# Performance work log

Measured on AMD Instinct MI355X. Metric: run time of the kernel, lower is better.

Reference implementation:

```python
import jax, jax.numpy as jnp
import numpy as np

B, CIN, COUT, H, W = 8, 128, 256, 64, 64
EPS = 1e-5


def conv2d(x, w, b, pad):
    y = jax.lax.conv_general_dilated(
        x, w, window_strides=(1, 1), padding=[(pad, pad), (pad, pad)],
        dimension_numbers=('NCHW', 'OIHW', 'NCHW'))
    return y + b[None, :, None, None]


def deform_sample(x, offset):
    # x: [B,C,H,W], offset: [B,18,H,W] -> sampled: [B,C,9,H,W]
    b, c, h, w = x.shape
    off = offset.reshape(b, 9, 2, h, w)  # (dy, dx) per kernel tap (torchvision v1 order)
    ky = (jnp.arange(9) // 3 - 1).astype(x.dtype)
    kx = (jnp.arange(9) % 3 - 1).astype(x.dtype)
    py = jnp.arange(h, dtype=x.dtype)[None, None, :, None] + ky[None, :, None, None] + off[:, :, 0]
    px = jnp.arange(w, dtype=x.dtype)[None, None, None, :] + kx[None, :, None, None] + off[:, :, 1]
    y0 = jnp.floor(py); x0 = jnp.floor(px)
    fy = py - y0;       fx = px - x0
    xf = x.reshape(b, c, h * w)

    def gather(iy, ix):
        valid = (iy >= 0) & (iy < h) & (ix >= 0) & (ix < w)
        iyc = jnp.clip(iy, 0, h - 1).astype(jnp.int32)
        ixc = jnp.clip(ix, 0, w - 1).astype(jnp.int32)
        idx = (iyc * w + ixc).reshape(b, -1)  # [B, 9*H*W]
        g = jax.vmap(lambda xb, ib: jnp.take(xb, ib, axis=1))(xf, idx)  # [B,C,9HW]
        return g.reshape(b, c, 9, h, w) * valid.astype(x.dtype)[:, None]

    samp = (gather(y0,     x0    ) * ((1 - fy) * (1 - fx))[:, None]
          + gather(y0,     x0 + 1) * ((1 - fy) * fx      )[:, None]
          + gather(y0 + 1, x0    ) * (fy * (1 - fx)      )[:, None]
          + gather(y0 + 1, x0 + 1) * (fy * fx            )[:, None])
    return samp


def setup_inputs():
    key = jax.random.key(0)
    ks = jax.random.split(key, 8)
    return {
        'x':     jax.random.normal(ks[0], (B, CIN, H, W), jnp.float32),
        'w_off': jax.random.normal(ks[1], (18, CIN, 3, 3), jnp.float32) * 0.01,
        'b_off': jnp.zeros((18,), jnp.float32),
        'w_def': jax.random.normal(ks[2], (COUT, CIN, 3, 3), jnp.float32) * 0.03,
        'b_def': jax.random.normal(ks[3], (COUT,), jnp.float32) * 0.01,
        'gamma': jnp.ones((COUT,), jnp.float32),
        'beta':  jnp.zeros((COUT,), jnp.float32),
        'w_sc':  jax.random.normal(ks[4], (COUT, CIN, 1, 1), jnp.float32) * 0.05,
        'b_sc':  jnp.zeros((COUT,), jnp.float32),
    }


def reference(x, w_off, b_off, w_def, b_def, gamma, beta, w_sc, b_sc):
    offset = conv2d(x, w_off, b_off, pad=1)                 # [B,18,H,W]
    samp = deform_sample(x, offset)                         # [B,C,9,H,W]
    out = jnp.einsum('bckhw,ock->bohw', samp, w_def.reshape(COUT, CIN, 9))
    out = out + b_def[None, :, None, None]
    # BatchNorm2d (training mode: batch statistics)
    mean = out.mean(axis=(0, 2, 3))
    var = out.var(axis=(0, 2, 3))
    out = (out - mean[None, :, None, None]) * jax.lax.rsqrt(var + EPS)[None, :, None, None]
    out = out * gamma[None, :, None, None] + beta[None, :, None, None]
    out = out + conv2d(x, w_sc, b_sc, pad=0)                # residual shortcut (1x1)
    return jax.nn.relu(out)
```

## Files before the change

kernel.cpp:

```cpp
#include <hip/hip_runtime.h>

typedef __attribute__((ext_vector_type(8))) short bf16x8;
typedef __attribute__((ext_vector_type(4))) float f32x4;

__device__ __forceinline__ float bf2f(unsigned short u) {
  return __uint_as_float(((unsigned int)u) << 16);
}
__device__ __forceinline__ unsigned short f2bf(float f) {
  unsigned int u = __float_as_uint(f);
  u += 0x7fffu + ((u >> 16) & 1u);
  return (unsigned short)(u >> 16);
}

constexpr size_t OFF_XPAD = 0;
constexpr size_t SZ_XPAD  = (size_t)8 * 66 * 66 * 128 * 2;
constexpr size_t OFF_WB   = OFF_XPAD + SZ_XPAD;
constexpr size_t SZ_WB    = (size_t)9 * 16 * 256 * 8 * 2;
constexpr size_t OFF_WS2  = OFF_WB + SZ_WB;
constexpr size_t SZ_WS2   = (size_t)16 * 256 * 8 * 2;
constexpr size_t OFF_WO   = OFF_WS2 + SZ_WS2;
constexpr size_t SZ_WO    = (size_t)9 * 16 * 32 * 8 * 2;
constexpr size_t OFF_OFFS = OFF_WO + SZ_WO;
constexpr size_t SZ_OFFS  = (size_t)9 * 32768 * 2 * 4;
constexpr size_t OFF_YM   = OFF_OFFS + SZ_OFFS;
constexpr size_t SZ_YM    = (size_t)32768 * 256 * 2;
constexpr size_t OFF_PART = OFF_YM + SZ_YM;
constexpr size_t SZ_PART  = (size_t)512 * 256 * 2 * 4;
constexpr size_t OFF_STAT = OFF_PART + SZ_PART;

__global__ __launch_bounds__(256) void k_prep_x(const float* __restrict__ x,
                                                unsigned short* __restrict__ xp) {
  int blk = blockIdx.x;
  int b = blk >> 6, h = blk & 63;
  int t = threadIdx.x;
  __shared__ float tile[16][66];
  for (int cc = 0; cc < 8; ++cc) {
    int c0 = cc * 16;
    int wr = t & 63, cl = t >> 6;
#pragma unroll
    for (int i = 0; i < 4; ++i) {
      int c = c0 + cl * 4 + i;
      tile[cl * 4 + i][wr] = x[(((size_t)b * 128 + c) * 64 + h) * 64 + wr];
    }
    __syncthreads();
    int ww = t >> 2, cq = t & 3;
    ushort4 u4;
    u4.x = f2bf(tile[cq * 4 + 0][ww]);
    u4.y = f2bf(tile[cq * 4 + 1][ww]);
    u4.z = f2bf(tile[cq * 4 + 2][ww]);
    u4.w = f2bf(tile[cq * 4 + 3][ww]);
    *(ushort4*)(xp + ((size_t)(b * 66 + h + 1) * 66 + (ww + 1)) * 128 + c0 + cq * 4) = u4;
    __syncthreads();
  }
}

__global__ __launch_bounds__(256) void k_pack_w(const float* __restrict__ wdef,
                                                const float* __restrict__ wsc,
                                                const float* __restrict__ woff,
                                                unsigned short* __restrict__ wB,
                                                unsigned short* __restrict__ wS,
                                                unsigned short* __restrict__ wO) {
  int tid = blockIdx.x * 256 + threadIdx.x;
  if (tid < 294912) {
    int k8 = tid & 7, n = (tid >> 3) & 255, kb = (tid >> 11) & 15, tap = tid >> 15;
    int c = kb * 8 + k8;
    wB[tid] = f2bf(wdef[((size_t)n * 128 + c) * 9 + tap]);
  } else if (tid < 294912 + 32768) {
    int i = tid - 294912;
    int k8 = i & 7, n = (i >> 3) & 255, kb = i >> 11;
    wS[i] = f2bf(wsc[(size_t)n * 128 + kb * 8 + k8]);
  } else if (tid < 294912 + 32768 + 36864) {
    int i = tid - 327680;
    int k8 = i & 7, n = (i >> 3) & 31, kb = (i >> 8) & 15, tap = i >> 12;
    int c = kb * 8 + k8;
    wO[i] = f2bf(n < 18 ? woff[((size_t)n * 128 + c) * 9 + tap] : 0.f);
  }
}

__global__ __launch_bounds__(256) void k_offset(const unsigned short* __restrict__ xp,
                                                const unsigned short* __restrict__ wO,
                                                const float* __restrict__ boff,
                                                float* __restrict__ offs) {
  int blk = blockIdx.x;
  int b = blk >> 6, h = blk & 63;
  int t = threadIdx.x;
  int lane = t & 63, wid = t >> 6;
  int m = lane & 15, quad = lane >> 4;
  f32x4 acc0 = {0.f, 0.f, 0.f, 0.f}, acc1 = {0.f, 0.f, 0.f, 0.f};
  int px = wid * 16 + m;
  const unsigned short* xbase = xp + ((size_t)(b * 66 + h) * 66 + px) * 128 + quad * 8;
  for (int tap = 0; tap < 9; ++tap) {
    int ty = tap / 3, tx = tap % 3;
    const unsigned short* arow = xbase + (ty * 66 + tx) * 128;
#pragma unroll
    for (int kk = 0; kk < 4; ++kk) {
      bf16x8 a = *(const bf16x8*)(arow + kk * 32);
      const unsigned short* bb = wO + (size_t)(tap * 16 + kk * 4 + quad) * 32 * 8;
      bf16x8 b0 = *(const bf16x8*)(bb + m * 8);
      bf16x8 b1 = *(const bf16x8*)(bb + (16 + m) * 8);
      acc0 = __builtin_amdgcn_mfma_f32_16x16x32_bf16(a, b0, acc0, 0, 0, 0);
      acc1 = __builtin_amdgcn_mfma_f32_16x16x32_bf16(a, b1, acc1, 0, 0, 0);
    }
  }
#pragma unroll
  for (int r = 0; r < 4; ++r) {
    int pxs = wid * 16 + quad * 4 + r;
    int pg = blk * 64 + pxs;
    offs[((size_t)(m >> 1) * 32768 + pg) * 2 + (m & 1)] = acc0[r] + boff[m];
    if (m < 2)
      offs[((size_t)8 * 32768 + pg) * 2 + m] = acc1[r] + boff[16 + m];
  }
}

__global__ __launch_bounds__(256) void k_main(const unsigned short* __restrict__ xp,
                                              const unsigned short* __restrict__ wB,
                                              const float* __restrict__ offs,
                                              const float* __restrict__ bdef,
                                              unsigned short* __restrict__ ymain,
                                              float* __restrict__ partials) {
  int blk = blockIdx.x;
  int b = blk >> 6, h = blk & 63;
  int t = threadIdx.x;
  int lane = t & 63, wid = t >> 6;
  int m = lane & 15, quad = lane >> 4;
  __shared__ __align__(16) unsigned short At[2][64 * 136];

  f32x4 acc[4][4];
#pragma unroll
  for (int i = 0; i < 4; ++i)
#pragma unroll
    for (int j = 0; j < 4; ++j) acc[i][j] = (f32x4){0.f, 0.f, 0.f, 0.f};

  int spx = t & 63, cg = t >> 6;
  int pg = blk * 64 + spx;
  float2 offv[9];
#pragma unroll
  for (int tap = 0; tap < 9; ++tap)
    offv[tap] = ((const float2*)offs)[(size_t)tap * 32768 + pg];

  const unsigned short* xb_base = xp + (size_t)b * 66 * 66 * 128 + cg * 32;
  int nb = wid * 64;

  auto sample_prep = [&](int tap, float* wgt, const unsigned short** p) {
    int ky = tap / 3 - 1, kx = tap % 3 - 1;
    float py = (float)(h + ky) + offv[tap].x;
    float pxf = (float)(spx + kx) + offv[tap].y;
    float y0f = floorf(py), x0f = floorf(pxf);
    float fy = py - y0f, fx = pxf - x0f;
    int iy0 = (int)y0f, ix0 = (int)x0f;
#pragma unroll
    for (int j = 0; j < 4; ++j) {
      int iy = iy0 + (j >> 1), ix = ix0 + (j & 1);
      float wy = (j >> 1) ? fy : 1.f - fy;
      float wx = (j & 1) ? fx : 1.f - fx;
      bool valid = (iy >= 0) && (iy < 64) && (ix >= 0) && (ix < 64);
      int iyc = min(max(iy, 0), 63), ixc = min(max(ix, 0), 63);
      wgt[j] = valid ? wy * wx : 0.f;
      p[j] = xb_base + ((size_t)(iyc + 1) * 66 + (ixc + 1)) * 128;
    }
  };
  auto load_half = [&](const unsigned short** p, int c0, bf16x8 (*v)[4]) {
#pragma unroll
    for (int cc = 0; cc < 2; ++cc)
#pragma unroll
      for (int j = 0; j < 4; ++j)
        v[cc][j] = *(const bf16x8*)(p[j] + (c0 + cc) * 8);
  };
  auto store_half = [&](unsigned short* dst, int c0, const float* wgt, bf16x8 (*v)[4]) {
#pragma unroll
    for (int cc = 0; cc < 2; ++cc) {
      bf16x8 o;
#pragma unroll
      for (int j = 0; j < 8; ++j) {
        float s = fmaf(wgt[0], bf2f((unsigned short)v[cc][0][j]),
                  fmaf(wgt[1], bf2f((unsigned short)v[cc][1][j]),
                  fmaf(wgt[2], bf2f((unsigned short)v[cc][2][j]),
                       wgt[3] * bf2f((unsigned short)v[cc][3][j]))));
        o[j] = (short)f2bf(s);
      }
      *(bf16x8*)(dst + (c0 + cc) * 8) = o;
    }
  };
  auto mfma_half = [&](const unsigned short* buf, int tap, int kk0) {
#pragma unroll
    for (int kk = kk0; kk < kk0 + 2; ++kk) {
      bf16x8 af[4];
#pragma unroll
      for (int ms = 0; ms < 4; ++ms)
        af[ms] = *(const bf16x8*)(buf + (ms * 16 + m) * 136 + kk * 32 + quad * 8);
#pragma unroll
      for (int ns = 0; ns < 4; ++ns) {
        bf16x8 bfr = *(const bf16x8*)(wB + ((size_t)(tap * 16 + kk * 4 + quad) * 256 + nb + ns * 16 + m) * 8);
#pragma unroll
        for (int ms = 0; ms < 4; ++ms)
          acc[ms][ns] = __builtin_amdgcn_mfma_f32_16x16x32_bf16(af[ms], bfr, acc[ms][ns], 0, 0, 0);
      }
    }
  };

  {
    float wgt[4]; const unsigned short* p[4]; bf16x8 v[2][4];
    sample_prep(0, wgt, p);
    unsigned short* dst = &At[0][spx * 136 + cg * 32];
    load_half(p, 0, v); store_half(dst, 0, wgt, v);
    load_half(p, 2, v); store_half(dst, 2, wgt, v);
  }
#pragma unroll
  for (int tap = 0; tap < 9; ++tap) {
    __syncthreads();
    const unsigned short* cur = At[tap & 1];
    unsigned short* dst = &At[(tap + 1) & 1][spx * 136 + cg * 32];
    if (tap < 8) {
      float wgt[4]; const unsigned short* p[4]; bf16x8 v[2][4];
      sample_prep(tap + 1, wgt, p);
      load_half(p, 0, v);
      mfma_half(cur, tap, 0);
      store_half(dst, 0, wgt, v);
      load_half(p, 2, v);
      mfma_half(cur, tap, 2);
      store_half(dst, 2, wgt, v);
    } else {
      mfma_half(cur, tap, 0);
      mfma_half(cur, tap, 2);
    }
  }

#pragma unroll
  for (int ns = 0; ns < 4; ++ns) {
    int n = nb + ns * 16 + m;
    float bias = bdef[n];
    float s = 0.f, q = 0.f;
#pragma unroll
    for (int ms = 0; ms < 4; ++ms) {
#pragma unroll
      for (int r = 0; r < 4; ++r) {
        int px = ms * 16 + quad * 4 + r;
        float v = acc[ms][ns][r] + bias;
        ymain[(size_t)(blk * 64 + px) * 256 + n] = f2bf(v);
        s += v;
        q += v * v;
      }
    }
    s += __shfl_xor(s, 16); s += __shfl_xor(s, 32);
    q += __shfl_xor(q, 16); q += __shfl_xor(q, 32);
    if (quad == 0) {
      partials[((size_t)blk * 256 + n) * 2 + 0] = s;
      partials[((size_t)blk * 256 + n) * 2 + 1] = q;
    }
  }
}

__global__ __launch_bounds__(64) void k_stats(const float* __restrict__ partials,
                                              const float* __restrict__ gamma,
                                              const float* __restrict__ beta,
                                              float* __restrict__ stats) {
  int ch = blockIdx.x;
  int L = threadIdx.x;
  float s = 0.f, q = 0.f;
#pragma unroll
  for (int i = 0; i < 8; ++i) {
    int row = i * 64 + L;
    s += partials[((size_t)row * 256 + ch) * 2 + 0];
    q += partials[((size_t)row * 256 + ch) * 2 + 1];
  }
#pragma unroll
  for (int d = 1; d < 64; d <<= 1) { s += __shfl_xor(s, d); q += __shfl_xor(q, d); }
  if (L == 0) {
    float mean = s * (1.f / 32768.f);
    float var = q * (1.f / 32768.f) - mean * mean;
    float inv = rsqrtf(var + 1e-5f);
    float A = gamma[ch] * inv;
    stats[ch * 2 + 0] = A;
    stats[ch * 2 + 1] = beta[ch] - mean * A;
  }
}

__global__ __launch_bounds__(256) void k_final(const unsigned short* __restrict__ xp,
                                               const unsigned short* __restrict__ wS,
                                               const unsigned short* __restrict__ ymain,
                                               const float* __restrict__ stats,
                                               const float* __restrict__ bsc,
                                               float* __restrict__ out) {
  int blk = blockIdx.x;
  int b = blk >> 6, h = blk & 63;
  int t = threadIdx.x;
  int lane = t & 63, wid = t >> 6;
  int m = lane & 15, quad = lane >> 4;
  __shared__ float tr[128 * 67];
  f32x4 acc[4][4];
#pragma unroll
  for (int i = 0; i < 4; ++i)
#pragma unroll
    for (int j = 0; j < 4; ++j) acc[i][j] = (f32x4){0.f, 0.f, 0.f, 0.f};
  const unsigned short* xrow = xp + ((size_t)(b * 66 + h + 1) * 66 + 1) * 128;
  int nb = wid * 64;
#pragma unroll
  for (int kk = 0; kk < 4; ++kk) {
    bf16x8 af[4];
#pragma unroll
    for (int ms = 0; ms < 4; ++ms)
      af[ms] = *(const bf16x8*)(xrow + (ms * 16 + m) * 128 + kk * 32 + quad * 8);
#pragma unroll
    for (int ns = 0; ns < 4; ++ns) {
      bf16x8 bfr = *(const bf16x8*)(wS + ((size_t)(kk * 4 + quad) * 256 + nb + ns * 16 + m) * 8);
#pragma unroll
      for (int ms = 0; ms < 4; ++ms)
        acc[ms][ns] = __builtin_amdgcn_mfma_f32_16x16x32_bf16(af[ms], bfr, acc[ms][ns], 0, 0, 0);
    }
  }
  for (int pass = 0; pass < 2; ++pass) {
    if ((wid >> 1) == pass) {
#pragma unroll
      for (int ns = 0; ns < 4; ++ns) {
        int n = nb + ns * 16 + m;
        float bs = bsc[n];
        int nl = n - pass * 128;
#pragma unroll
        for (int ms = 0; ms < 4; ++ms)
#pragma unroll
          for (int r = 0; r < 4; ++r) {
            int px = ms * 16 + quad * 4 + r;
            tr[nl * 67 + px] = acc[ms][ns][r] + bs;
          }
      }
    }
    __syncthreads();
    {
      int nl = t & 127, g = t >> 7;
      int n = pass * 128 + nl;
      float A = stats[n * 2], Bc = stats[n * 2 + 1];
#pragma unroll 8
      for (int i = 0; i < 32; ++i) {
        int px = g * 32 + i;
        float ym = bf2f(ymain[(size_t)(blk * 64 + px) * 256 + n]);
        float* pt = &tr[nl * 67 + px];
        *pt = fmaxf(fmaf(ym, A, Bc) + *pt, 0.f);
      }
    }
    __syncthreads();
    {
      int ww = t & 63, ng = t >> 6;
#pragma unroll 8
      for (int i = 0; i < 32; ++i) {
        int nl = ng * 32 + i;
        out[((size_t)(b * 256 + pass * 128 + nl) * 64 + h) * 64 + ww] = tr[nl * 67 + ww];
      }
    }
    __syncthreads();
  }
}

extern "C" void kernel_launch(void* const* d_in, const int* in_sizes, int n_in,
                              void* d_out, int out_size, void* d_ws, size_t ws_size,
                              hipStream_t stream) {
  const float* x     = (const float*)d_in[0];
  const float* w_off = (const float*)d_in[1];
  const float* b_off = (const float*)d_in[2];
  const float* w_def = (const float*)d_in[3];
  const float* b_def = (const float*)d_in[4];
  const float* gamma = (const float*)d_in[5];
  const float* beta  = (const float*)d_in[6];
  const float* w_sc  = (const float*)d_in[7];
  const float* b_sc  = (const float*)d_in[8];
  float* out = (float*)d_out;

  char* ws = (char*)d_ws;
  unsigned short* xpad  = (unsigned short*)(ws + OFF_XPAD);
  unsigned short* wB    = (unsigned short*)(ws + OFF_WB);
  unsigned short* wS    = (unsigned short*)(ws + OFF_WS2);
  unsigned short* wO    = (unsigned short*)(ws + OFF_WO);
  float* offs           = (float*)(ws + OFF_OFFS);
  unsigned short* ymain = (unsigned short*)(ws + OFF_YM);
  float* partials       = (float*)(ws + OFF_PART);
  float* stats          = (float*)(ws + OFF_STAT);

  hipMemsetAsync(xpad, 0, SZ_XPAD, stream);
  k_prep_x<<<512, 256, 0, stream>>>(x, xpad);
  k_pack_w<<<1424, 256, 0, stream>>>(w_def, w_sc, w_off, wB, wS, wO);
  k_offset<<<512, 256, 0, stream>>>(xpad, wO, b_off, offs);
  k_main<<<512, 256, 0, stream>>>(xpad, wB, offs, b_def, ymain, partials);
  k_stats<<<256, 64, 0, stream>>>(partials, gamma, beta, stats);
  k_final<<<512, 256, 0, stream>>>(xpad, wS, ymain, stats, b_sc, out);
}
```

Baseline: 182.9 us.

## Fuse offset conv into main deform kernel, remap sampling threads, stage output in LDS

The offset convolution is computed inside the main kernel, and its results go to shared memory rather than a global buffer, which removes a kernel launch and the global round trip for offsets. The sampling thread mapping changes so four adjacent threads share a pixel and read interleaved 8-channel chunks, which should coalesce the bilinear gathers better. The bf16 main output is staged through LDS and written as contiguous 16-byte rows instead of scattered 2-byte stores. In exchange, each block now recomputes offsets serially before its main loop and uses more LDS, which may lower occupancy.

Result: faster. 162.1 us (-11.3%).

```diff
diff --git a/kernel.cpp b/kernel.cpp
--- a/kernel.cpp
+++ b/kernel.cpp
@@ -20,9 +20,7 @@
 constexpr size_t SZ_WS2   = (size_t)16 * 256 * 8 * 2;
 constexpr size_t OFF_WO   = OFF_WS2 + SZ_WS2;
 constexpr size_t SZ_WO    = (size_t)9 * 16 * 32 * 8 * 2;
-constexpr size_t OFF_OFFS = OFF_WO + SZ_WO;
-constexpr size_t SZ_OFFS  = (size_t)9 * 32768 * 2 * 4;
-constexpr size_t OFF_YM   = OFF_OFFS + SZ_OFFS;
+constexpr size_t OFF_YM   = OFF_WO + SZ_WO;
 constexpr size_t SZ_YM    = (size_t)32768 * 256 * 2;
 constexpr size_t OFF_PART = OFF_YM + SZ_YM;
 constexpr size_t SZ_PART  = (size_t)512 * 256 * 2 * 4;
@@ -77,44 +75,10 @@
   }
 }
 
-__global__ __launch_bounds__(256) void k_offset(const unsigned short* __restrict__ xp,
-                                                const unsigned short* __restrict__ wO,
-                                                const float* __restrict__ boff,
-                                                float* __restrict__ offs) {
-  int blk = blockIdx.x;
-  int b = blk >> 6, h = blk & 63;
-  int t = threadIdx.x;
-  int lane = t & 63, wid = t >> 6;
-  int m = lane & 15, quad = lane >> 4;
-  f32x4 acc0 = {0.f, 0.f, 0.f, 0.f}, acc1 = {0.f, 0.f, 0.f, 0.f};
-  int px = wid * 16 + m;
-  const unsigned short* xbase = xp + ((size_t)(b * 66 + h) * 66 + px) * 128 + quad * 8;
-  for (int tap = 0; tap < 9; ++tap) {
-    int ty = tap / 3, tx = tap % 3;
-    const unsigned short* arow = xbase + (ty * 66 + tx) * 128;
-#pragma unroll
-    for (int kk = 0; kk < 4; ++kk) {
-      bf16x8 a = *(const bf16x8*)(arow + kk * 32);
-      const unsigned short* bb = wO + (size_t)(tap * 16 + kk * 4 + quad) * 32 * 8;
-      bf16x8 b0 = *(const bf16x8*)(bb + m * 8);
-      bf16x8 b1 = *(const bf16x8*)(bb + (16 + m) * 8);
-      acc0 = __builtin_amdgcn_mfma_f32_16x16x32_bf16(a, b0, acc0, 0, 0, 0);
-      acc1 = __builtin_amdgcn_mfma_f32_16x16x32_bf16(a, b1, acc1, 0, 0, 0);
-    }
-  }
-#pragma unroll
-  for (int r = 0; r < 4; ++r) {
-    int pxs = wid * 16 + quad * 4 + r;
-    int pg = blk * 64 + pxs;
-    offs[((size_t)(m >> 1) * 32768 + pg) * 2 + (m & 1)] = acc0[r] + boff[m];
-    if (m < 2)
-      offs[((size_t)8 * 32768 + pg) * 2 + m] = acc1[r] + boff[16 + m];
-  }
-}
-
 __global__ __launch_bounds__(256) void k_main(const unsigned short* __restrict__ xp,
                                               const unsigned short* __restrict__ wB,
-                                              const float* __restrict__ offs,
+                                              const unsigned short* __restrict__ wO,
+                                              const float* __restrict__ boff,
                                               const float* __restrict__ bdef,
                                               unsigned short* __restrict__ ymain,
                                               float* __restrict__ partials) {
@@ -124,6 +88,32 @@
   int lane = t & 63, wid = t >> 6;
   int m = lane & 15, quad = lane >> 4;
   __shared__ __align__(16) unsigned short At[2][64 * 136];
+  __shared__ float offsL[9][64][2];
+
+  {
+    f32x4 a0 = {0.f, 0.f, 0.f, 0.f}, a1 = {0.f, 0.f, 0.f, 0.f};
+    int px = wid * 16 + m;
+    const unsigned short* xbase = xp + ((size_t)(b * 66 + h) * 66 + px) * 128 + quad * 8;
+    for (int tap = 0; tap < 9; ++tap) {
+      const unsigned short* arow = xbase + ((tap / 3) * 66 + (tap % 3)) * 128;
+#pragma unroll
+      for (int kk = 0; kk < 4; ++kk) {
+        bf16x8 a = *(const bf16x8*)(arow + kk * 32);
+        const unsigned short* bb = wO + (size_t)(tap * 16 + kk * 4 + quad) * 256;
+        bf16x8 b0 = *(const bf16x8*)(bb + m * 8);
+        bf16x8 b1 = *(const bf16x8*)(bb + (16 + m) * 8);
+        a0 = __builtin_amdgcn_mfma_f32_16x16x32_bf16(a, b0, a0, 0, 0, 0);
+        a1 = __builtin_amdgcn_mfma_f32_16x16x32_bf16(a, b1, a1, 0, 0, 0);
+      }
+    }
+#pragma unroll
+    for (int r = 0; r < 4; ++r) {
+      int pxs = wid * 16 + quad * 4 + r;
+      offsL[m >> 1][pxs][m & 1] = a0[r] + boff[m];
+      if (m < 2) offsL[8][pxs][m] = a1[r] + boff[16 + m];
+    }
+  }
+  __syncthreads();
 
   f32x4 acc[4][4];
 #pragma unroll
@@ -131,20 +121,15 @@
 #pragma unroll
     for (int j = 0; j < 4; ++j) acc[i][j] = (f32x4){0.f, 0.f, 0.f, 0.f};
 
-  int spx = t & 63, cg = t >> 6;
-  int pg = blk * 64 + spx;
-  float2 offv[9];
-#pragma unroll
-  for (int tap = 0; tap < 9; ++tap)
-    offv[tap] = ((const float2*)offs)[(size_t)tap * 32768 + pg];
-
-  const unsigned short* xb_base = xp + (size_t)b * 66 * 66 * 128 + cg * 32;
+  int px_s = t >> 2, sub = t & 3;
+  const unsigned short* xb_base = xp + (size_t)b * 66 * 66 * 128;
   int nb = wid * 64;
 
   auto sample_prep = [&](int tap, float* wgt, const unsigned short** p) {
+    float2 ov = *(const float2*)&offsL[tap][px_s][0];
     int ky = tap / 3 - 1, kx = tap % 3 - 1;
-    float py = (float)(h + ky) + offv[tap].x;
-    float pxf = (float)(spx + kx) + offv[tap].y;
+    float py = (float)(h + ky) + ov.x;
+    float pxf = (float)(px_s + kx) + ov.y;
     float y0f = floorf(py), x0f = floorf(pxf);
     float fy = py - y0f, fx = pxf - x0f;
     int iy0 = (int)y0f, ix0 = (int)x0f;
@@ -156,29 +141,29 @@
       bool valid = (iy >= 0) && (iy < 64) && (ix >= 0) && (ix < 64);
       int iyc = min(max(iy, 0), 63), ixc = min(max(ix, 0), 63);
       wgt[j] = valid ? wy * wx : 0.f;
-      p[j] = xb_base + ((size_t)(iyc + 1) * 66 + (ixc + 1)) * 128;
+      p[j] = xb_base + ((size_t)(iyc + 1) * 66 + (ixc + 1)) * 128 + sub * 8;
     }
   };
-  auto load_half = [&](const unsigned short** p, int c0, bf16x8 (*v)[4]) {
-#pragma unroll
-    for (int cc = 0; cc < 2; ++cc)
+  auto load_g2 = [&](const unsigned short** p, int g0, bf16x8 (*v)[4]) {
+#pragma unroll
+    for (int gg = 0; gg < 2; ++gg)
 #pragma unroll
       for (int j = 0; j < 4; ++j)
-        v[cc][j] = *(const bf16x8*)(p[j] + (c0 + cc) * 8);
+        v[gg][j] = *(const bf16x8*)(p[j] + (g0 + gg) * 32);
   };
-  auto store_half = [&](unsigned short* dst, int c0, const float* wgt, bf16x8 (*v)[4]) {
-#pragma unroll
-    for (int cc = 0; cc < 2; ++cc) {
+  auto store_g2 = [&](unsigned short* dst, int g0, const float* wgt, bf16x8 (*v)[4]) {
+#pragma unroll
+    for (int gg = 0; gg < 2; ++gg) {
       bf16x8 o;
 #pragma unroll
       for (int j = 0; j < 8; ++j) {
-        float s = fmaf(wgt[0], bf2f((unsigned short)v[cc][0][j]),
-                  fmaf(wgt[1], bf2f((unsigned short)v[cc][1][j]),
-                  fmaf(wgt[2], bf2f((unsigned short)v[cc][2][j]),
-                       wgt[3] * bf2f((unsigned short)v[cc][3][j]))));
+        float s = fmaf(wgt[0], bf2f((unsigned short)v[gg][0][j]),
+                  fmaf(wgt[1], bf2f((unsigned short)v[gg][1][j]),
+                  fmaf(wgt[2], bf2f((unsigned short)v[gg][2][j]),
+                       wgt[3] * bf2f((unsigned short)v[gg][3][j]))));
         o[j] = (short)f2bf(s);
       }
-      *(bf16x8*)(dst + (c0 + cc) * 8) = o;
+      *(bf16x8*)(dst + (g0 + gg) * 32) = o;
     }
   };
   auto mfma_half = [&](const unsigned short* buf, int tap, int kk0) {
@@ -201,30 +186,32 @@
   {
     float wgt[4]; const unsigned short* p[4]; bf16x8 v[2][4];
     sample_prep(0, wgt, p);
-    unsigned short* dst = &At[0][spx * 136 + cg * 32];
-    load_half(p, 0, v); store_half(dst, 0, wgt, v);
-    load_half(p, 2, v); store_half(dst, 2, wgt, v);
+    unsigned short* dst = &At[0][px_s * 136 + sub * 8];
+    load_g2(p, 0, v); store_g2(dst, 0, wgt, v);
+    load_g2(p, 2, v); store_g2(dst, 2, wgt, v);
   }
 #pragma unroll
   for (int tap = 0; tap < 9; ++tap) {
     __syncthreads();
     const unsigned short* cur = At[tap & 1];
-    unsigned short* dst = &At[(tap + 1) & 1][spx * 136 + cg * 32];
+    unsigned short* dst = &At[(tap + 1) & 1][px_s * 136 + sub * 8];
     if (tap < 8) {
       float wgt[4]; const unsigned short* p[4]; bf16x8 v[2][4];
       sample_prep(tap + 1, wgt, p);
-      load_half(p, 0, v);
+      load_g2(p, 0, v);
       mfma_half(cur, tap, 0);
-      store_half(dst, 0, wgt, v);
-      load_half(p, 2, v);
+      store_g2(dst, 0, wgt, v);
+      load_g2(p, 2, v);
       mfma_half(cur, tap, 2);
-      store_half(dst, 2, wgt, v);
+      store_g2(dst, 2, wgt, v);
     } else {
       mfma_half(cur, tap, 0);
       mfma_half(cur, tap, 2);
     }
   }
 
+  __syncthreads();
+  unsigned short* yb = &At[0][0];
 #pragma unroll
   for (int ns = 0; ns < 4; ++ns) {
     int n = nb + ns * 16 + m;
@@ -236,7 +223,7 @@
       for (int r = 0; r < 4; ++r) {
         int px = ms * 16 + quad * 4 + r;
         float v = acc[ms][ns][r] + bias;
-        ymain[(size_t)(blk * 64 + px) * 256 + n] = f2bf(v);
+        yb[px * 264 + n] = f2bf(v);
         s += v;
         q += v * v;
       }
@@ -246,6 +233,16 @@
     if (quad == 0) {
       partials[((size_t)blk * 256 + n) * 2 + 0] = s;
       partials[((size_t)blk * 256 + n) * 2 + 1] = q;
+    }
+  }
+  __syncthreads();
+  {
+    unsigned short* grow = ymain + (size_t)(blk * 64 + px_s) * 256;
+    const unsigned short* lrow = yb + px_s * 264;
+#pragma unroll
+    for (int k = 0; k < 8; ++k) {
+      int n0 = k * 32 + sub * 8;
+      *(bf16x8*)(grow + n0) = *(const bf16x8*)(lrow + n0);
     }
   }
 }
@@ -369,7 +366,6 @@
   unsigned short* wB    = (unsigned short*)(ws + OFF_WB);
   unsigned short* wS    = (unsigned short*)(ws + OFF_WS2);
   unsigned short* wO    = (unsigned short*)(ws + OFF_WO);
-  float* offs           = (float*)(ws + OFF_OFFS);
   unsigned short* ymain = (unsigned short*)(ws + OFF_YM);
   float* partials       = (float*)(ws + OFF_PART);
   float* stats          = (float*)(ws + OFF_STAT);
@@ -377,8 +373,7 @@
   hipMemsetAsync(xpad, 0, SZ_XPAD, stream);
   k_prep_x<<<512, 256, 0, stream>>>(x, xpad);
   k_pack_w<<<1424, 256, 0, stream>>>(w_def, w_sc, w_off, wB, wS, wO);
-  k_offset<<<512, 256, 0, stream>>>(xpad, wO, b_off, offs);
-  k_main<<<512, 256, 0, stream>>>(xpad, wB, offs, b_def, ymain, partials);
+  k_main<<<512, 256, 0, stream>>>(xpad, wB, wO, b_off, b_def, ymain, partials);
   k_stats<<<256, 64, 0, stream>>>(partials, gamma, beta, stats);
   k_final<<<512, 256, 0, stream>>>(xpad, wS, ymain, stats, b_sc, out);
 }
```
